# Kernel tuning notes

Hardware: AMD Instinct MI355X
Metric: run time of the kernel (lower is better)

Reference implementation:

```python
import jax, jax.numpy as jnp
import numpy as np

SEQ = 256  # position axis length fixed by the graph's iota(256)


def _mod(freq, phase):
    # sin(2*pi*t*freq + phase)^2 * 0.1 + 1 - 0.05, shape [SEQ]
    t = jnp.arange(SEQ, dtype=jnp.float32)
    return jnp.sin(t * (2.0 * jnp.pi) * freq + phase) ** 2 * 0.1 + 0.95


def setup_inputs() -> dict:
    key = jax.random.key(0)
    ks = jax.random.split(key, 16)
    K = 2048  # number of scattered index triples
    return {
        "primals_1": jax.random.normal(ks[0], (6, 256, 256), jnp.float32),
        "primals_2": jax.random.normal(ks[1], (12, 6, 256), jnp.float32),
        "primals_3": jax.random.normal(ks[2], (6, 256, 256), jnp.float32),
        "primals_4": jax.random.normal(ks[3], (6, 256), jnp.float32),
        "primals_5": jax.random.randint(ks[4], (K,), 0, 6),
        "primals_6": jax.random.randint(ks[5], (K,), 0, 256),
        "primals_7": jax.random.randint(ks[6], (K,), 0, 256),
        "primals_8": jax.random.randint(ks[7], (K,), 0, 256),
        "primals_9": jax.random.uniform(ks[8], (1,), jnp.float32),
        "primals_10": jax.random.uniform(ks[9], (1,), jnp.float32),
        "primals_11": jax.random.normal(ks[10], (6, 256), jnp.float32),
        "primals_12": jax.random.uniform(ks[11], (1,), jnp.float32),
        "primals_13": jax.random.uniform(ks[12], (1,), jnp.float32),
        "primals_14": jax.random.normal(ks[13], (6, 256), jnp.float32),
        "primals_15": jax.random.uniform(ks[14], (1,), jnp.float32),
        "primals_16": jax.random.uniform(ks[15], (1,), jnp.float32),
    }


def reference(primals_1, primals_2, primals_3, primals_4, primals_5, primals_6,
              primals_7, primals_8, primals_9, primals_10, primals_11, primals_12,
              primals_13, primals_14, primals_15, primals_16):
    decay = primals_3 * 0.975  # reused in all three stages

    def stage(q, table, freq, phase):
        # gather from table [6,256] at (p5,p6) -> [K]
        vals = table[primals_5, primals_6]
        # scatter into a fresh copy of the persistent buffer, then decay-accumulate
        mem = primals_1.at[primals_5, primals_7, primals_8].set(vals) + decay  # [6,256,256]
        # bmm 'attention': q [12,6,256] x mem [6,256,256] -> [12,6,256]
        att = jnp.einsum('hbd,bde->hbe', q, mem)
        return att, _mod(freq, phase)

    a1, m1 = stage(primals_2, primals_4, primals_9, primals_10)
    x1 = a1 / m1
    a2, m2 = stage(x1, primals_11, primals_12, primals_13)
    x2 = a2 * m2
    a3, m3 = stage(x2, primals_14, primals_15, primals_16)
    return a3 / m3
```

## Files before the change

kernel.cpp:

```cpp
#include <hip/hip_runtime.h>

#define TWO_PI 6.2831853071795864769f

__global__ __launch_bounds__(1024, 4) void fused_chain(
    const float* __restrict__ P1, const float* __restrict__ P2,
    const float* __restrict__ P3, const float* __restrict__ T4,
    const int* __restrict__ p5, const int* __restrict__ p6,
    const int* __restrict__ p7, const int* __restrict__ p8,
    const float* __restrict__ f1, const float* __restrict__ ph1,
    const float* __restrict__ T11, const float* __restrict__ f2,
    const float* __restrict__ ph2, const float* __restrict__ T14,
    const float* __restrict__ f3, const float* __restrict__ ph3,
    float* __restrict__ out, int K)
{
    const int blk = (int)blockIdx.x;
    const int b = blk & 7;
    if (b >= 6) return;
    const int h = blk >> 3;

    __shared__ float v[256];
    __shared__ float pv[16][256];
    __shared__ float modl[3][256];
    __shared__ unsigned hmap[4096];
    __shared__ unsigned short wde[2048];
    __shared__ float wv0[2048], wv1[2048], wv2[2048];
    __shared__ int nw;

    const int tid = (int)threadIdx.x;
    const int dg = tid >> 6;
    const int eg = tid & 63;
    const int start = (h * 16) / 12;

    const float4* P1v = (const float4*)P1;
    const float4* P3v = (const float4*)P3;
    float4 m4[16];
    #pragma unroll
    for (int j = 0; j < 16; ++j) {
        int sl = (j + start) & 15;
        int row = (b << 8) + (sl << 4) + dg;
        float4 a = P1v[row * 64 + eg];
        float4 c = P3v[row * 64 + eg];
        m4[j].x = fmaf(c.x, 0.975f, a.x);
        m4[j].y = fmaf(c.y, 0.975f, a.y);
        m4[j].z = fmaf(c.z, 0.975f, a.z);
        m4[j].w = fmaf(c.w, 0.975f, a.w);
    }

    if (tid < 256) v[tid] = P2[(h * 6 + b) * 256 + tid];
    if (tid < 768) {
        int s = tid >> 8, ee = tid & 255;
        float fr = (s == 0) ? f1[0]  : (s == 1) ? f2[0]  : f3[0];
        float ph = (s == 0) ? ph1[0] : (s == 1) ? ph2[0] : ph3[0];
        float sn = __sinf((float)ee * TWO_PI * fr + ph);
        float mm = sn * sn * 0.1f + 0.95f;
        modl[s][ee] = (s == 1) ? mm : 1.0f / mm;
    }
    for (int i = tid; i < 4096; i += 1024) hmap[i] = 0xFFFFFFFFu;
    if (tid == 0) nw = 0;
    __syncthreads();

    for (int k = tid; k < K; k += 1024) {
        if (p5[k] != b) continue;
        unsigned key = ((unsigned)p7[k] << 8) | (unsigned)p8[k];
        unsigned mine = (key << 12) | (unsigned)k;
        unsigned hh = (key * 2654435761u) >> 20;
        for (;;) {
            unsigned prev = atomicCAS(&hmap[hh], 0xFFFFFFFFu, mine);
            if (prev == 0xFFFFFFFFu) break;
            if ((prev >> 12) == key) { atomicMax(&hmap[hh], mine); break; }
            hh = (hh + 1) & 4095u;
        }
    }
    __syncthreads();

    for (int k = tid; k < K; k += 1024) {
        if (p5[k] != b) continue;
        unsigned key = ((unsigned)p7[k] << 8) | (unsigned)p8[k];
        unsigned hh = (key * 2654435761u) >> 20;
        unsigned cur;
        for (;;) {
            cur = hmap[hh];
            if ((cur >> 12) == key) break;
            hh = (hh + 1) & 4095u;
        }
        if ((cur & 0xFFFu) == (unsigned)k) {
            int c = p6[k];
            float p1v = P1[(b << 16) | key];
            int w = atomicAdd(&nw, 1);
            wde[w] = (unsigned short)key;
            wv0[w] = T4 [b * 256 + c] - p1v;
            wv1[w] = T11[b * 256 + c] - p1v;
            wv2[w] = T14[b * 256 + c] - p1v;
        }
    }
    __syncthreads();
    const int nwl = nw;

    const int e256 = tid & 255;
    for (int s = 0; s < 3; ++s) {
        float4 acc = make_float4(0.f, 0.f, 0.f, 0.f);
        #pragma unroll
        for (int j = 0; j < 16; ++j) {
            float vv = v[(((j + start) & 15) << 4) + dg];
            acc.x = fmaf(vv, m4[j].x, acc.x);
            acc.y = fmaf(vv, m4[j].y, acc.y);
            acc.z = fmaf(vv, m4[j].z, acc.z);
            acc.w = fmaf(vv, m4[j].w, acc.w);
        }
        *(float4*)&pv[dg][eg << 2] = acc;
        __syncthreads();
        {
            int r = tid >> 8;
            float x = pv[r][e256] + pv[r + 4][e256] +
                      pv[r + 8][e256] + pv[r + 12][e256];
            __syncthreads();
            pv[r][e256] = x;
        }
        __syncthreads();
        if (tid < 256)
            pv[0][tid] = (pv[0][tid] + pv[1][tid]) + (pv[2][tid] + pv[3][tid]);
        __syncthreads();
        const float* wvs = (s == 0) ? wv0 : (s == 1) ? wv1 : wv2;
        for (int i = tid; i < nwl; i += 1024) {
            unsigned de = wde[i];
            atomicAdd(&pv[0][de & 255u], v[de >> 8] * wvs[i]);
        }
        __syncthreads();
        if (tid < 256)
            v[tid] = pv[0][tid] * modl[s][tid];
        __syncthreads();
    }
    if (tid < 256) out[(h * 6 + b) * 256 + tid] = v[tid];
}

extern "C" void kernel_launch(void* const* d_in, const int* in_sizes, int n_in,
                              void* d_out, int out_size, void* d_ws, size_t ws_size,
                              hipStream_t stream)
{
    (void)n_in; (void)out_size; (void)d_ws; (void)ws_size;
    const float* P1  = (const float*)d_in[0];
    const float* P2  = (const float*)d_in[1];
    const float* P3  = (const float*)d_in[2];
    const float* T4  = (const float*)d_in[3];
    const int*   p5  = (const int*)d_in[4];
    const int*   p6  = (const int*)d_in[5];
    const int*   p7  = (const int*)d_in[6];
    const int*   p8  = (const int*)d_in[7];
    const float* f1  = (const float*)d_in[8];
    const float* ph1 = (const float*)d_in[9];
    const float* T11 = (const float*)d_in[10];
    const float* f2  = (const float*)d_in[11];
    const float* ph2 = (const float*)d_in[12];
    const float* T14 = (const float*)d_in[13];
    const float* f3  = (const float*)d_in[14];
    const float* ph3 = (const float*)d_in[15];
    float* out = (float*)d_out;
    int K = in_sizes[4];

    hipLaunchKernelGGL(fused_chain, dim3(96), dim3(1024), 0, stream,
                       P1, P2, P3, T4, p5, p6, p7, p8,
                       f1, ph1, T11, f2, ph2, T14, f3, ph3, out, K);
}
```

Baseline: 21.84 us.

## Stream P1/P3 tiles through LDS with double-buffered async global_load_lds

Replaces the direct per-thread float4 loads of P1 and P3 into registers with a double-buffered pipeline that uses global_load_lds to copy 16-row chunks into shared memory, waits with explicit vmcnt and barriers, then reads from LDS. It also drops the per-head staggered start offset and aliases the hash map with the partial-sum buffer to offset the added LDS use. The aim is to keep more loads in flight and overlap them with the FMA work. The cost is two block-wide barriers per chunk and much higher LDS use, which may reduce how many blocks fit on a CU.

```diff
diff --git a/kernel.cpp b/kernel.cpp
--- a/kernel.cpp
+++ b/kernel.cpp
@@ -18,10 +18,11 @@
     if (b >= 6) return;
     const int h = blk >> 3;
 
+    __shared__ float sP1[2][4096];
+    __shared__ float sP3[2][4096];
     __shared__ float v[256];
-    __shared__ float pv[16][256];
+    __shared__ unsigned hmap_pv[4096];
     __shared__ float modl[3][256];
-    __shared__ unsigned hmap[4096];
     __shared__ unsigned short wde[2048];
     __shared__ float wv0[2048], wv1[2048], wv2[2048];
     __shared__ int nw;
@@ -29,22 +30,43 @@
     const int tid = (int)threadIdx.x;
     const int dg = tid >> 6;
     const int eg = tid & 63;
-    const int start = (h * 16) / 12;
+    const int lane4 = eg << 2;
 
-    const float4* P1v = (const float4*)P1;
-    const float4* P3v = (const float4*)P3;
     float4 m4[16];
+    #define ISSUE_CHUNK(c, buf)                                               \
+        do {                                                                  \
+            const float* g1 = P1 + ((((b << 8) + ((c) << 4) + dg)) << 8) + lane4; \
+            const float* g3 = P3 + ((((b << 8) + ((c) << 4) + dg)) << 8) + lane4; \
+            __builtin_amdgcn_global_load_lds(                                 \
+                (const __attribute__((address_space(1))) void*)g1,            \
+                (__attribute__((address_space(3))) void*)&sP1[buf][dg << 8],  \
+                16, 0, 0);                                                    \
+            __builtin_amdgcn_global_load_lds(                                 \
+                (const __attribute__((address_space(1))) void*)g3,            \
+                (__attribute__((address_space(3))) void*)&sP3[buf][dg << 8],  \
+                16, 0, 0);                                                    \
+        } while (0)
+
+    ISSUE_CHUNK(0, 0);
+    ISSUE_CHUNK(1, 1);
     #pragma unroll
-    for (int j = 0; j < 16; ++j) {
-        int sl = (j + start) & 15;
-        int row = (b << 8) + (sl << 4) + dg;
-        float4 a = P1v[row * 64 + eg];
-        float4 c = P3v[row * 64 + eg];
-        m4[j].x = fmaf(c.x, 0.975f, a.x);
-        m4[j].y = fmaf(c.y, 0.975f, a.y);
-        m4[j].z = fmaf(c.z, 0.975f, a.z);
-        m4[j].w = fmaf(c.w, 0.975f, a.w);
+    for (int c = 0; c < 16; ++c) {
+        if (c == 15) asm volatile("s_waitcnt vmcnt(0)" ::: "memory");
+        else         asm volatile("s_waitcnt vmcnt(4)" ::: "memory");
+        __builtin_amdgcn_sched_barrier(0);
+        __builtin_amdgcn_s_barrier();
+        float4 a = *(const float4*)&sP1[c & 1][(dg << 8) + lane4];
+        float4 p = *(const float4*)&sP3[c & 1][(dg << 8) + lane4];
+        m4[c].x = fmaf(p.x, 0.975f, a.x);
+        m4[c].y = fmaf(p.y, 0.975f, a.y);
+        m4[c].z = fmaf(p.z, 0.975f, a.z);
+        m4[c].w = fmaf(p.w, 0.975f, a.w);
+        asm volatile("s_waitcnt lgkmcnt(0)" ::: "memory");
+        __builtin_amdgcn_sched_barrier(0);
+        __builtin_amdgcn_s_barrier();
+        if (c + 2 < 16) ISSUE_CHUNK(c + 2, c & 1);
     }
+    #undef ISSUE_CHUNK
 
     if (tid < 256) v[tid] = P2[(h * 6 + b) * 256 + tid];
     if (tid < 768) {
@@ -55,7 +77,7 @@
         float mm = sn * sn * 0.1f + 0.95f;
         modl[s][ee] = (s == 1) ? mm : 1.0f / mm;
     }
-    for (int i = tid; i < 4096; i += 1024) hmap[i] = 0xFFFFFFFFu;
+    for (int i = tid; i < 4096; i += 1024) hmap_pv[i] = 0xFFFFFFFFu;
     if (tid == 0) nw = 0;
     __syncthreads();
 
@@ -65,9 +87,9 @@
         unsigned mine = (key << 12) | (unsigned)k;
         unsigned hh = (key * 2654435761u) >> 20;
         for (;;) {
-            unsigned prev = atomicCAS(&hmap[hh], 0xFFFFFFFFu, mine);
+            unsigned prev = atomicCAS(&hmap_pv[hh], 0xFFFFFFFFu, mine);
             if (prev == 0xFFFFFFFFu) break;
-            if ((prev >> 12) == key) { atomicMax(&hmap[hh], mine); break; }
+            if ((prev >> 12) == key) { atomicMax(&hmap_pv[hh], mine); break; }
             hh = (hh + 1) & 4095u;
         }
     }
@@ -79,7 +101,7 @@
         unsigned hh = (key * 2654435761u) >> 20;
         unsigned cur;
         for (;;) {
-            cur = hmap[hh];
+            cur = hmap_pv[hh];
             if ((cur >> 12) == key) break;
             hh = (hh + 1) & 4095u;
         }
@@ -96,18 +118,19 @@
     __syncthreads();
     const int nwl = nw;
 
+    float (*pv)[256] = (float(*)[256])hmap_pv;
     const int e256 = tid & 255;
     for (int s = 0; s < 3; ++s) {
         float4 acc = make_float4(0.f, 0.f, 0.f, 0.f);
         #pragma unroll
         for (int j = 0; j < 16; ++j) {
-            float vv = v[(((j + start) & 15) << 4) + dg];
+            float vv = v[(j << 4) + dg];
             acc.x = fmaf(vv, m4[j].x, acc.x);
             acc.y = fmaf(vv, m4[j].y, acc.y);
             acc.z = fmaf(vv, m4[j].z, acc.z);
             acc.w = fmaf(vv, m4[j].w, acc.w);
         }
-        *(float4*)&pv[dg][eg << 2] = acc;
+        *(float4*)&pv[dg][lane4] = acc;
         __syncthreads();
         {
             int r = tid >> 8;
```

Result: slower. 24.52 us (+12.2%).
